# Kernel optimization log

Measured on AMD Instinct MI355X. Metric: run time of the kernel, lower is better.

Reference implementation:

```python
import jax, jax.numpy as jnp
import numpy as np

IMG = 224; P = 16; C_IN = 3; D = 768; DEPTH = 12; H = 12; HD = D // H
MLP = 4 * D; NCLS = 1000
GRID = IMG // P; NPATCH = GRID * GRID; N = NPATCH + 1
NRD = (2 * GRID - 1) * (2 * GRID - 1) + 3  # num_relative_distance


def _rel_pos_index():
    # replicates the torch buffer construction (BEiT-style)
    coords = np.stack(np.meshgrid(np.arange(GRID), np.arange(GRID), indexing='ij')).reshape(2, -1)
    rel = (coords[:, :, None] - coords[:, None, :]).transpose(1, 2, 0).astype(np.int64)
    rel[:, :, 0] += GRID - 1
    rel[:, :, 1] += GRID - 1
    rel[:, :, 0] *= 2 * GRID - 1
    idx = np.zeros((N, N), dtype=np.int64)
    idx[1:, 1:] = rel.sum(-1)
    idx[0, :] = NRD - 3
    idx[:, 0] = NRD - 2
    idx[0, 0] = NRD - 1
    return jnp.asarray(idx)

REL_IDX = _rel_pos_index()  # [N, N] int


def setup_inputs() -> dict:
    key = jax.random.key(0)
    ks = jax.random.split(key, 12)
    r = lambda k, shp: jax.random.normal(k, shp, jnp.float32) * 0.02
    return {
        'x': jax.random.normal(ks[0], (32, C_IN, IMG, IMG), jnp.float32),
        'patch_w': r(ks[1], (D, C_IN * P * P)),
        'patch_b': jnp.zeros((D,), jnp.float32),
        'cls_token': r(ks[2], (1, 1, D)),
        'pos_embed': r(ks[3], (1, N, D)),
        'norm1_s': jnp.ones((DEPTH, D), jnp.float32),
        'norm1_b': jnp.zeros((DEPTH, D), jnp.float32),
        'qkv_w': r(ks[4], (DEPTH, 3 * D, D)),
        'q_bias': jnp.zeros((DEPTH, D), jnp.float32),
        'v_bias': jnp.zeros((DEPTH, D), jnp.float32),
        'rpb_table': r(ks[5], (DEPTH, NRD, H)),
        'proj_w': r(ks[6], (DEPTH, D, D)),
        'proj_b': jnp.zeros((DEPTH, D), jnp.float32),
        'norm2_s': jnp.ones((DEPTH, D), jnp.float32),
        'norm2_b': jnp.zeros((DEPTH, D), jnp.float32),
        'fc1_w': r(ks[7], (DEPTH, MLP, D)),
        'fc1_b': jnp.zeros((DEPTH, MLP), jnp.float32),
        'fc2_w': r(ks[8], (DEPTH, D, MLP)),
        'fc2_b': jnp.zeros((DEPTH, D), jnp.float32),
        'gamma1': jnp.full((DEPTH, D), 0.1, jnp.float32),
        'gamma2': jnp.full((DEPTH, D), 0.1, jnp.float32),
        'normf_s': jnp.ones((D,), jnp.float32),
        'normf_b': jnp.zeros((D,), jnp.float32),
        'head_w': r(ks[9], (NCLS, D)),
        'head_b': jnp.zeros((NCLS,), jnp.float32),
    }


def _ln(x, s, b):
    m = jnp.mean(x, -1, keepdims=True)
    v = jnp.mean((x - m) ** 2, -1, keepdims=True)
    return (x - m) * jax.lax.rsqrt(v + 1e-5) * s + b


def reference(x, patch_w, patch_b, cls_token, pos_embed, norm1_s, norm1_b, qkv_w,
              q_bias, v_bias, rpb_table, proj_w, proj_b, norm2_s, norm2_b,
              fc1_w, fc1_b, fc2_w, fc2_b, gamma1, gamma2, normf_s, normf_b,
              head_w, head_b):
    B = x.shape[0]
    # Patch embed: stride=kernel conv == unfold + matmul
    t = x.reshape(B, C_IN, GRID, P, GRID, P).transpose(0, 2, 4, 1, 3, 5).reshape(B, NPATCH, C_IN * P * P)
    t = t @ patch_w.T + patch_b                                   # [B, 196, D]
    t = jnp.concatenate([jnp.broadcast_to(cls_token, (B, 1, D)), t], axis=1) + pos_embed
    scale = HD ** -0.5
    for i in range(DEPTH):
        h = _ln(t, norm1_s[i], norm1_b[i])
        qkv_b = jnp.concatenate([q_bias[i], jnp.zeros_like(q_bias[i]), v_bias[i]])
        qkv = (h @ qkv_w[i].T + qkv_b).reshape(B, N, 3, H, HD)
        q = qkv[:, :, 0].transpose(0, 2, 1, 3)                    # [B, H, N, HD]
        k = qkv[:, :, 1].transpose(0, 2, 1, 3)
        v = qkv[:, :, 2].transpose(0, 2, 1, 3)
        bias = rpb_table[i][REL_IDX].transpose(2, 0, 1)           # [H, N, N]
        attn = jax.nn.softmax(jnp.einsum('bhqd,bhkd->bhqk', q * scale, k) + bias[None], axis=-1)
        o = jnp.einsum('bhqk,bhkd->bhqd', attn, v).transpose(0, 2, 1, 3).reshape(B, N, D)
        t = t + gamma1[i] * (o @ proj_w[i].T + proj_b[i])
        h2 = _ln(t, norm2_s[i], norm2_b[i])
        m = jax.nn.gelu(h2 @ fc1_w[i].T + fc1_b[i], approximate=False) @ fc2_w[i].T + fc2_b[i]
        t = t + gamma2[i] * m
    t = _ln(t, normf_s, normf_b)
    return t[:, 0] @ head_w.T + head_b                            # [B, NCLS]
```

## Files before the change

### kernel.cpp

```cpp
#include <hip/hip_runtime.h>
#include <hip/hip_bf16.h>


typedef __hip_bfloat16 bf16s;
using bf16x8 = __attribute__((ext_vector_type(8))) __bf16;
using f32x4  = __attribute__((ext_vector_type(4))) float;

#define DEV static __device__ __forceinline__

DEV float b2f(bf16s x) { return __bfloat162float(x); }
DEV bf16s f2b(float x) { return __float2bfloat16(x); }

DEV void gload_lds16(const void* g, void* l) {
  __builtin_amdgcn_global_load_lds((const __attribute__((address_space(1))) void*)g,
                                   (__attribute__((address_space(3))) void*)l, 16, 0, 0);
}

constexpr int B_   = 32;
constexpr int H_   = 12;
constexpr int NTOK = 197;
constexpr int NPAD = 224;
constexpr int MVALP= 6272;
constexpr int MVAL = B_*NTOK;
constexpr int MROW = 6400;
constexpr int MLP_ = 3072;
constexpr int BH   = B_*H_;
constexpr int NRD  = 732;
constexpr int NNP  = 224*224;

constexpr size_t OFF_T   = 0;
constexpr size_t SZ_T    = (size_t)MROW*768*4;
constexpr size_t OFF_H   = OFF_T + SZ_T;
constexpr size_t SZ_H    = (size_t)MROW*768*2;
constexpr size_t OFF_Q   = OFF_H + SZ_H;
constexpr size_t SZ_QKB  = (size_t)BH*NPAD*64*2;
constexpr size_t OFF_K   = OFF_Q + SZ_QKB;
constexpr size_t OFF_VT  = OFF_K + SZ_QKB;
constexpr size_t OFF_P   = OFF_VT + SZ_QKB;
constexpr size_t SZ_P    = (size_t)MROW*MLP_*2;
constexpr size_t OFF_O   = OFF_P + SZ_P;
constexpr size_t OFF_BT  = OFF_O + SZ_H;
constexpr size_t SZ_BT   = (size_t)12*H_*NNP*2;
constexpr size_t OFF_HF  = OFF_BT + SZ_BT;
constexpr size_t OFF_WB  = OFF_HF + 49152;
constexpr size_t WS_NEED = OFF_WB + (size_t)7077888*2;

constexpr size_t WB_QKV = 0;
constexpr size_t WB_PROJ= (size_t)2304*768;
constexpr size_t WB_FC1 = WB_PROJ + (size_t)768*768;
constexpr size_t WB_FC2 = WB_FC1 + (size_t)MLP_*768;

template<int MODE>
__global__ __launch_bounds__(512, 4)
void gemm8p(const bf16s* __restrict__ A, const bf16s* __restrict__ Bw,
            const int K, const int ldc,
            bf16s* __restrict__ Cb,
            const float* __restrict__ e0, const float* __restrict__ e1,
            float* __restrict__ tres,
            bf16s* __restrict__ qp, bf16s* __restrict__ kp, bf16s* __restrict__ vp)
{
  __shared__ bf16s lds[32768];
  const int tid  = threadIdx.x;
  const int lane = tid & 63;
  const int wid  = tid >> 6;
  const int wm   = wid >> 2, wn = wid & 3;

  const int ncols = gridDim.y;
  const int nwg = (int)gridDim.x * ncols;
  const int lin = (int)blockIdx.y * gridDim.x + blockIdx.x;
  const int xcd = lin & 7, pos = lin >> 3;
  const int q8 = nwg >> 3, r8 = nwg & 7;
  const int vid = (xcd < r8) ? xcd*(q8+1) + pos : r8*(q8+1) + (xcd-r8)*q8 + pos;
  constexpr int NBG = (MODE == 0) ? 6 : 8;
  const int gsz = NBG * (int)gridDim.x;
  const int g   = vid / gsz;
  const int rr  = vid - g*gsz;
  const int bm  = rr / NBG;
  const int bn  = g*NBG + (rr - bm*NBG);

  const int srow = (wid << 3) + (lane >> 3);
  const int colg = (((lane & 7) ^ (srow & 7)) << 3);
  const bf16s* gA = A  + (size_t)(bm*128 + srow)*K + colg;
  const bf16s* gB = Bw + (size_t)(bn*128 + srow)*K + colg;
  const size_t rK64 = (size_t)64*K;

  const int r15  = lane & 15;
  const int colr = (lane >> 4) << 3;
  const int exor = (lane & 7) << 3;
  const int ardA = wm*4096 + r15*64;
  const int ardB = 8192 + (wn*32 + r15)*64;

  f32x4 acc[4][2] = {};
  const int J = K >> 7;

#define STGA(h, kt, dbuf) do { \
    const bf16s* _g = gA + (size_t)(h)*rK64 + (size_t)(kt)*64; \
    gload_lds16(_g, &lds[(dbuf)*16384 + (h)*4096 + wid*512 + lane*8]); } while(0)
#define STGB(h, kt, dbuf) do { \
    const bf16s* _g = gB + (size_t)(h)*rK64 + (size_t)(kt)*64; \
    gload_lds16(_g, &lds[(dbuf)*16384 + 8192 + (h)*4096 + wid*512 + lane*8]); } while(0)

  STGB(0,0,0); STGB(1,0,0);
  STGA(0,0,0); STGA(1,0,0);
  STGB(0,1,1); STGB(1,1,1);

  bf16x8 bfr[2][2];

  for (int j = 0; j < J; ++j) {
    const bool more = (j+1 < J);
#pragma unroll
    for (int p = 0; p < 4; ++p) {
      __builtin_amdgcn_sched_barrier(0);
      if (p == 0) {
        asm volatile("s_waitcnt vmcnt(2)" ::: "memory");
      } else if (p == 2) {
        if (j+1 == J) asm volatile("s_waitcnt vmcnt(0)" ::: "memory");
        else          asm volatile("s_waitcnt vmcnt(2)" ::: "memory");
      }
      __builtin_amdgcn_sched_barrier(0);
      __builtin_amdgcn_s_barrier();
      __builtin_amdgcn_sched_barrier(0);

      if (p == 0)      { STGA(0, 2*j+1, 1); STGA(1, 2*j+1, 1); }
      else if (p == 1) { if (more) { STGB(0, 2*j+2, 0); STGB(1, 2*j+2, 0); } }
      else if (p == 2) { if (more) { STGA(0, 2*j+2, 0); STGA(1, 2*j+2, 0); } }
      else             { if (more) { STGB(0, 2*j+3, 1); STGB(1, 2*j+3, 1); } }

      const int d = (p < 2) ? 0 : 1;
      const int dbase = d*16384;
      const int q0 = (p & 1) << 1;
      if ((p & 1) == 0) {
#pragma unroll
        for (int nf=0; nf<2; nf++)
#pragma unroll
          for (int kss=0; kss<2; kss++)
            bfr[nf][kss] = *(const bf16x8*)&lds[dbase + ardB + nf*1024 + (((kss<<5) + colr) ^ exor)];
      }
      bf16x8 a1[2][2];
#pragma unroll
      for (int qq=0; qq<2; qq++)
#pragma unroll
        for (int kss=0; kss<2; kss++)
          a1[qq][kss] = *(const bf16x8*)&lds[dbase + ardA + (q0+qq)*1024 + (((kss<<5) + colr) ^ exor)];
      __builtin_amdgcn_s_setprio(1);
#pragma unroll
      for (int qq=0; qq<2; qq++)
#pragma unroll
        for (int nf=0; nf<2; nf++)
#pragma unroll
          for (int kss=0; kss<2; kss++)
            acc[q0+qq][nf] = __builtin_amdgcn_mfma_f32_16x16x32_bf16(a1[qq][kss], bfr[nf][kss], acc[q0+qq][nf], 0, 0, 0);
      __builtin_amdgcn_s_setprio(0);
    }
  }
#undef STGA
#undef STGB

  const int crow0 = (lane >> 4) * 4;

  if (MODE == 5) {
    __syncthreads();
#pragma unroll
    for (int mf = 0; mf < 4; ++mf)
#pragma unroll
      for (int nf = 0; nf < 2; ++nf)
#pragma unroll
        for (int r = 0; r < 4; ++r) {
          const int lrow = wm*64 + mf*16 + crow0 + r;
          const int lcol = wn*32 + nf*16 + r15;
          const float xx = acc[mf][nf][r] + e0[bn*128 + lcol];
          lds[lrow*136 + lcol] = f2b(0.5f*xx*(1.0f + erff(xx*0.70710678118654752f)));
        }
    __syncthreads();
#pragma unroll
    for (int it = 0; it < 4; ++it) {
      const int sid = it*512 + tid;
      const int row = sid >> 4, cg = sid & 15;
      const int grow = bm*128 + row;
      *(uint4*)&Cb[(size_t)grow*ldc + bn*128 + cg*8] =
          *(const uint4*)&lds[row*136 + cg*8];
    }
    return;
  }

  if (MODE == 0 && bn >= 12) {
    float* lf = (float*)lds;
    __syncthreads();
#pragma unroll
    for (int mf = 0; mf < 4; ++mf)
#pragma unroll
      for (int nf = 0; nf < 2; ++nf)
#pragma unroll
        for (int r = 0; r < 4; ++r) {
          const int col = wn*32 + nf*16 + r15;
          const int row = wm*64 + mf*16 + crow0 + r;
          lf[col*128 + (row ^ (col & 31))] = acc[mf][nf][r];
        }
    __syncthreads();
    const int rem0 = bn*128 - 1536;
#pragma unroll
    for (int ci = 0; ci < 16; ++ci) {
      const int c = wid*16 + ci;
      const int rem = rem0 + c;
      const int hh = rem >> 6, dd = rem & 63;
      const float vb = e1[rem];
      bf16s* vrow = vp + ((size_t)hh*64 + dd)*NPAD;
#pragma unroll
      for (int hf2 = 0; hf2 < 2; ++hf2) {
        const int row = hf2*64 + lane;
        const int grow = bm*128 + row;
        if (grow < MVAL) {
          const int b2 = grow/197, ntok = grow - b2*197;
          vrow[(size_t)b2*H_*64*NPAD + ntok] = f2b(lf[c*128 + (row ^ (c & 31))] + vb);
        }
      }
    }
    return;
  }

  if (MODE == 0) {
    const bool isq = (bn < 6);
    __syncthreads();
#pragma unroll
    for (int mf = 0; mf < 4; ++mf)
#pragma unroll
      for (int nf = 0; nf < 2; ++nf)
#pragma unroll
        for (int r = 0; r < 4; ++r) {
          const int lrow = wm*64 + mf*16 + crow0 + r;
          const int lcol = wn*32 + nf*16 + r15;
          float v = acc[mf][nf][r];
          if (isq) v = (v + e0[bn*128 + lcol])*0.125f;
          lds[lrow*136 + lcol] = f2b(v);
        }
    __syncthreads();
    bf16s* outp = isq ? qp : kp;
#pragma unroll
    for (int it = 0; it < 4; ++it) {
      const int sid = it*512 + tid;
      const int row = sid >> 4, cg = sid & 15;
      const int grow = bm*128 + row;
      if (grow < MVAL) {
        const int bb_ = grow/197, ntok = grow - bb_*197;
        const int lcol = cg*8;
        const int rem = isq ? (bn*128 + lcol) : (bn*128 + lcol - 768);
        const int hh = rem >> 6, dd = rem & 63;
        *(uint4*)&outp[(((size_t)bb_*H_ + hh)*NPAD + ntok)*64 + dd] =
            *(const uint4*)&lds[row*136 + lcol];
      }
    }
  }
}

template<int MODE>
__global__ __launch_bounds__(256, 3)
void gemm64n(const bf16s* __restrict__ A, const bf16s* __restrict__ Bw,
             const int K, const int ldc, bf16s* __restrict__ Cb,
             const float* __restrict__ e0, const float* __restrict__ e1,
             float* __restrict__ tres)
{
  __shared__ bf16s lds[24576];
  const int tid  = threadIdx.x;
  const int lane = tid & 63;
  const int wid  = tid >> 6;
  const int wm   = wid >> 1, wn = wid & 1;

  const int ncols = gridDim.y;
  const int nwg = (int)gridDim.x * ncols;
  const int lin = (int)blockIdx.y * gridDim.x + blockIdx.x;
  const int xcd = lin & 7, pos = lin >> 3;
  const int q8 = nwg >> 3, r8 = nwg & 7;
  const int vid = (xcd < r8) ? xcd*(q8+1) + pos : r8*(q8+1) + (xcd-r8)*q8 + pos;
  const int bm = vid / ncols, bn = vid - bm*ncols;

  const int srow = tid >> 3;
  const int colg = (((tid & 7) ^ (srow & 7)) << 3);
  const bf16s* gA = A  + (size_t)(bm*128 + srow)*K + colg;
  const bf16s* gB = Bw + (size_t)(bn*64  + srow)*K + colg;
  const size_t rK32 = (size_t)32*K;

  const int r15  = lane & 15;
  const int colr = (lane >> 4) << 3;
  const int exor = (lane & 7) << 3;
  const int ardA = wm*4096 + r15*64;
  const int ardB = 8192 + (wn*32 + r15)*64;

  f32x4 acc[4][2] = {};
  const int J = K >> 7;

#define STGA2(h, kt, dbuf) do { \
    const bf16s* _g = gA + (size_t)(h)*rK32 + (size_t)(kt)*64; \
    gload_lds16(_g, &lds[(dbuf)*12288 + (h)*2048 + tid*8]); } while(0)
#define STGB2(h, kt, dbuf) do { \
    const bf16s* _g = gB + (size_t)(h)*rK32 + (size_t)(kt)*64; \
    gload_lds16(_g, &lds[(dbuf)*12288 + 8192 + (h)*2048 + tid*8]); } while(0)

  STGB2(0,0,0); STGB2(1,0,0);
  STGA2(0,0,0); STGA2(1,0,0); STGA2(2,0,0); STGA2(3,0,0);
  STGB2(0,1,1); STGB2(1,1,1);

  bf16x8 bfr[2][2];

  for (int j = 0; j < J; ++j) {
    const bool more = (j+1 < J);
#pragma unroll
    for (int p = 0; p < 4; ++p) {
      __builtin_amdgcn_sched_barrier(0);
      if (p == 0) {
        asm volatile("s_waitcnt vmcnt(2)" ::: "memory");
      } else if (p == 2) {
        if (j+1 == J) asm volatile("s_waitcnt vmcnt(0)" ::: "memory");
        else          asm volatile("s_waitcnt vmcnt(2)" ::: "memory");
      }
      __builtin_amdgcn_sched_barrier(0);
      __builtin_amdgcn_s_barrier();
      __builtin_amdgcn_sched_barrier(0);

      if (p == 0)      { STGA2(0, 2*j+1, 1); STGA2(1, 2*j+1, 1); STGA2(2, 2*j+1, 1); STGA2(3, 2*j+1, 1); }
      else if (p == 1) { if (more) { STGB2(0, 2*j+2, 0); STGB2(1, 2*j+2, 0); } }
      else if (p == 2) { if (more) { STGA2(0, 2*j+2, 0); STGA2(1, 2*j+2, 0); STGA2(2, 2*j+2, 0); STGA2(3, 2*j+2, 0); } }
      else             { if (more) { STGB2(0, 2*j+3, 1); STGB2(1, 2*j+3, 1); } }

      const int d = (p < 2) ? 0 : 1;
      const int dbase = d*12288;
      const int q0 = (p & 1) << 1;
      if ((p & 1) == 0) {
#pragma unroll
        for (int nf=0; nf<2; nf++)
#pragma unroll
          for (int kss=0; kss<2; kss++)
            bfr[nf][kss] = *(const bf16x8*)&lds[dbase + ardB + nf*1024 + (((kss<<5) + colr) ^ exor)];
      }
      bf16x8 a1[2][2];
#pragma unroll
      for (int qq=0; qq<2; qq++)
#pragma unroll
        for (int kss=0; kss<2; kss++)
          a1[qq][kss] = *(const bf16x8*)&lds[dbase + ardA + (q0+qq)*1024 + (((kss<<5) + colr) ^ exor)];
      __builtin_amdgcn_s_setprio(1);
#pragma unroll
      for (int qq=0; qq<2; qq++)
#pragma unroll
        for (int nf=0; nf<2; nf++)
#pragma unroll
          for (int kss=0; kss<2; kss++)
            acc[q0+qq][nf] = __builtin_amdgcn_mfma_f32_16x16x32_bf16(a1[qq][kss], bfr[nf][kss], acc[q0+qq][nf], 0, 0, 0);
      __builtin_amdgcn_s_setprio(0);
    }
  }
#undef STGA2
#undef STGB2

  const int crow0 = (lane >> 4) * 4;
#pragma unroll
  for (int mf = 0; mf < 4; ++mf) {
#pragma unroll
    for (int r = 0; r < 4; ++r) {
      const int grow = bm*128 + wm*64 + mf*16 + crow0 + r;
      {
        float* trow = tres + (size_t)grow*768;
#pragma unroll
        for (int nf = 0; nf < 2; ++nf) {
          const int gcol = bn*64 + wn*32 + nf*16 + r15;
          trow[gcol] += e1[gcol]*(acc[mf][nf][r] + e0[gcol]);
        }
      }
    }
  }
}

__global__ __launch_bounds__(256, 5)
void gemm64p(const bf16s* __restrict__ A, const bf16s* __restrict__ Bw,
             int K,
             const float* __restrict__ e0, const float* __restrict__ e1,
             float* __restrict__ tres)
{
  __shared__ bf16s As[2][64*32];
  __shared__ bf16s Bs[2][128*32];
  const int tid  = threadIdx.x;
  const int lane = tid & 63;
  const int wave = tid >> 6;

  const int ncols = gridDim.y;
  const int nwg = (int)gridDim.x * ncols;
  const int lin = (int)blockIdx.y * gridDim.x + blockIdx.x;
  const int xcd = lin & 7, pos = lin >> 3;
  const int q8 = nwg >> 3, r8 = nwg & 7;
  const int vid = (xcd < r8) ? xcd*(q8+1) + pos : r8*(q8+1) + (xcd-r8)*q8 + pos;
  const int bm = vid / ncols, bn = vid - bm*ncols;

  f32x4 acc[2][4] = {};

  const int sr4  = lane >> 2;
  const int scol = ((lane&3) ^ (sr4&3))*8;
  const bf16s* gA = A  + (size_t)(bm*64  + wave*16 + sr4)*K + scol;
  const bf16s* gB = Bw + (size_t)(bn*128 + wave*32 + sr4)*K + scol;
  const size_t b16 = (size_t)16*K;
  const int dA  = wave*512  + lane*8;
  const int dB0 = wave*1024 + lane*8, dB1 = dB0 + 512;

  const int fr  = lane & 15;
  const int rdk = (((lane>>4) ^ (lane&3)))*8;
  const int wr = wave >> 1, wc = wave & 1;
  const int abase = (wr*32 + fr)*32 + rdk;
  const int bbase = (wc*64 + fr)*32 + rdk;

  const int nk = K >> 5;
  gload_lds16(gA,       &As[0][dA]);
  gload_lds16(gB,       &Bs[0][dB0]);
  gload_lds16(gB + b16, &Bs[0][dB1]);

  int cur = 0;
  for (int kt = 0; kt < nk; ++kt) {
    __syncthreads();
    if (kt + 1 < nk) {
      const bf16s* ga = gA + (size_t)(kt+1)*32;
      const bf16s* gb = gB + (size_t)(kt+1)*32;
      gload_lds16(ga,       &As[cur^1][dA]);
      gload_lds16(gb,       &Bs[cur^1][dB0]);
      gload_lds16(gb + b16, &Bs[cur^1][dB1]);
    }
    bf16x8 af[2], bfr[4];
    af[0] = *(const bf16x8*)&As[cur][abase];
    af[1] = *(const bf16x8*)&As[cur][abase + 512];
#pragma unroll
    for (int n2=0;n2<4;n2++) bfr[n2] = *(const bf16x8*)&Bs[cur][bbase + n2*512];
#pragma unroll
    for (int m=0;m<2;m++)
#pragma unroll
      for (int n2=0;n2<4;n2++)
        acc[m][n2] = __builtin_amdgcn_mfma_f32_16x16x32_bf16(af[m], bfr[n2], acc[m][n2], 0, 0, 0);
    cur ^= 1;
  }

  const int crow0 = (lane>>4)*4;
#pragma unroll
  for (int m=0;m<2;m++) {
#pragma unroll
    for (int r=0;r<4;r++) {
      const int grow = bm*64 + wr*32 + m*16 + crow0 + r;
      if (grow >= MVALP) continue;
      const int bb_ = grow/196, p = grow - bb_*196;
      float* trow = tres + ((size_t)bb_*197 + 1 + p)*768;
      const float* prow = e1 + (size_t)(1+p)*768;
#pragma unroll
      for (int n2=0;n2<4;n2++) {
        const int gcol = bn*128 + wc*64 + n2*16 + fr;
        trow[gcol] = acc[m][n2][r] + e0[gcol] + prow[gcol];
      }
    }
  }
}

__global__ __launch_bounds__(256)
void f2b_k(const float* __restrict__ src, bf16s* __restrict__ dst, int n4)
{
  int id = blockIdx.x*256 + threadIdx.x;
  if (id >= n4) return;
  const float4 v = ((const float4*)src)[id];
  union { bf16s b[4]; uint2 u; } uu;
  uu.b[0] = f2b(v.x); uu.b[1] = f2b(v.y); uu.b[2] = f2b(v.z); uu.b[3] = f2b(v.w);
  ((uint2*)dst)[id] = uu.u;
}

__global__ __launch_bounds__(256)
void prep_k(const float* __restrict__ tin, const float* __restrict__ s,
            const float* __restrict__ b, bf16s* __restrict__ outp,
            const float* __restrict__ qw, const float* __restrict__ pw,
            const float* __restrict__ f1, const float* __restrict__ f2,
            bf16s* __restrict__ wb)
{
  const int tid = threadIdx.x;
  if (blockIdx.x < MVAL) {
    const int r = blockIdx.x;
    const float* xr = tin + (size_t)r*768;
    float v0 = xr[tid], v1 = xr[tid+256], v2 = xr[tid+512];
    float sum = v0+v1+v2;
#pragma unroll
    for (int off=32; off>=1; off>>=1) sum += __shfl_xor(sum, off, 64);
    __shared__ float red[8];
    const int wv = tid>>6, ln = tid&63;
    if (ln==0) red[wv] = sum;
    __syncthreads();
    const float mean = (red[0]+red[1]+red[2]+red[3]) * (1.0f/768.0f);
    const float d0=v0-mean, d1=v1-mean, d2=v2-mean;
    float sq = d0*d0 + d1*d1 + d2*d2;
#pragma unroll
    for (int off=32; off>=1; off>>=1) sq += __shfl_xor(sq, off, 64);
    if (ln==0) red[4+wv] = sq;
    __syncthreads();
    const float rs = rsqrtf((red[4]+red[5]+red[6]+red[7])*(1.0f/768.0f) + 1e-5f);
    bf16s* orow = outp + (size_t)r*768;
    orow[tid]     = f2b(d0*rs*s[tid]     + b[tid]);
    orow[tid+256] = f2b(d1*rs*s[tid+256] + b[tid+256]);
    orow[tid+512] = f2b(d2*rs*s[tid+512] + b[tid+512]);
  } else {
    int id = (blockIdx.x - MVAL)*256 + tid;
    const float* src; size_t dst; int loc;
    if (id < 442368)           { src = qw; loc = id;          dst = WB_QKV; }
    else if (id < 589824)      { src = pw; loc = id-442368;   dst = WB_PROJ; }
    else if (id < 1179648)     { src = f1; loc = id-589824;   dst = WB_FC1; }
    else                       { src = f2; loc = id-1179648;  dst = WB_FC2; }
    const float4 v = ((const float4*)src)[loc];
    union { bf16s bb[4]; uint2 u; } uu;
    uu.bb[0] = f2b(v.x); uu.bb[1] = f2b(v.y); uu.bb[2] = f2b(v.z); uu.bb[3] = f2b(v.w);
    ((uint2*)(wb + dst))[loc] = uu.u;
  }
}

__global__ __launch_bounds__(256)
void bias_all_k(const float* __restrict__ rpb, bf16s* __restrict__ biasT)
{
  int id = blockIdx.x*256 + threadIdx.x;
  if (id >= 12*H_*NNP) return;
  const int l   = id / (H_*NNP);
  const int r2  = id - l*(H_*NNP);
  const int hh  = r2 / NNP;
  const int rem = r2 - hh*NNP;
  int i = rem / 224, j = rem - i*224;
  if (i > 196) i = 196;
  if (j > 196) j = 196;
  int v;
  if (i==0 && j==0)      v = NRD-1;
  else if (i==0)         v = NRD-3;
  else if (j==0)         v = NRD-2;
  else {
    const int p = i-1, q = j-1;
    v = (p/14 - q/14 + 13)*27 + (p%14 - q%14 + 13);
  }
  biasT[id] = f2b(rpb[(size_t)l*NRD*H_ + v*H_ + hh]);
}

__global__ __launch_bounds__(256)
void im2col_k(const float* __restrict__ x, bf16s* __restrict__ pat)
{
  int id = blockIdx.x*256 + threadIdx.x;
  if (id >= MVALP*768) return;
  int col = id % 768;  int row = id / 768;
  int b = row / 196, p = row % 196;
  int gy = p / 14, gx = p % 14;
  int c = col >> 8, rem = col & 255, py = rem >> 4, px = rem & 15;
  pat[id] = f2b(x[ ((size_t)(b*3 + c)*224 + gy*16 + py)*224 + gx*16 + px ]);
}

__global__ __launch_bounds__(256)
void clspos_k(const float* __restrict__ cls, const float* __restrict__ pos, float* __restrict__ t)
{
  int id = blockIdx.x*256 + threadIdx.x;
  int d = id % 768, b = id / 768;
  t[(size_t)b*197*768 + d] = cls[d] + pos[d];
}

__global__ __launch_bounds__(256)
void ln_k(const float* __restrict__ tin, const float* __restrict__ s,
          const float* __restrict__ b, bf16s* __restrict__ outp, int instride)
{
  const int r = blockIdx.x, tid = threadIdx.x;
  const float* xr = tin + (size_t)r*instride;
  float v0 = xr[tid], v1 = xr[tid+256], v2 = xr[tid+512];
  float sum = v0+v1+v2;
#pragma unroll
  for (int off=32; off>=1; off>>=1) sum += __shfl_xor(sum, off, 64);
  __shared__ float red[8];
  const int wv = tid>>6, ln = tid&63;
  if (ln==0) red[wv] = sum;
  __syncthreads();
  const float mean = (red[0]+red[1]+red[2]+red[3]) * (1.0f/768.0f);
  const float d0=v0-mean, d1=v1-mean, d2=v2-mean;
  float sq = d0*d0 + d1*d1 + d2*d2;
#pragma unroll
  for (int off=32; off>=1; off>>=1) sq += __shfl_xor(sq, off, 64);
  if (ln==0) red[4+wv] = sq;
  __syncthreads();
  const float rs = rsqrtf((red[4]+red[5]+red[6]+red[7])*(1.0f/768.0f) + 1e-5f);
  bf16s* orow = outp + (size_t)r*768;
  orow[tid]     = f2b(d0*rs*s[tid]     + b[tid]);
  orow[tid+256] = f2b(d1*rs*s[tid+256] + b[tid+256]);
  orow[tid+512] = f2b(d2*rs*s[tid+512] + b[tid+512]);
}

__global__ __launch_bounds__(64)
void attn_fused(const bf16s* __restrict__ q, const bf16s* __restrict__ k,
                const bf16s* __restrict__ vT, const bf16s* __restrict__ biasT,
                bf16s* __restrict__ o)
{
  __shared__ bf16s Pl[32][232];
  const int gid = blockIdx.x;
  const int qt = gid % 7, bh = gid / 7;
  const int b = bh / H_, hh = bh % H_;
  const int lane = threadIdx.x;
  const int fr = lane & 15, fk = (lane>>4)*8;

  const bf16s* bTq = biasT + (size_t)hh*NNP + (size_t)(qt*32)*224;
#pragma unroll
  for (int rr = 0; rr < 32; ++rr) {
    if (lane < 28) gload_lds16(bTq + (size_t)rr*224 + lane*8, &Pl[rr][lane*8]);
  }

  const bf16s* qp = q + (size_t)bh*NPAD*64;
  const bf16s* kp = k + (size_t)bh*NPAD*64;
  bf16x8 a[2][2];
#pragma unroll
  for (int m=0;m<2;m++)
#pragma unroll
    for (int kk=0;kk<2;kk++)
      a[m][kk] = *(const bf16x8*)&qp[(qt*32 + m*16 + fr)*64 + kk*32 + fk];

  f32x4 acc[2][14] = {};
  __builtin_amdgcn_s_setprio(1);
#pragma unroll
  for (int nt=0; nt<14; nt++) {
    bf16x8 bb0 = *(const bf16x8*)&kp[(nt*16 + fr)*64 + fk];
    bf16x8 bb1 = *(const bf16x8*)&kp[(nt*16 + fr)*64 + 32 + fk];
    acc[0][nt] = __builtin_amdgcn_mfma_f32_16x16x32_bf16(a[0][0], bb0, acc[0][nt], 0,0,0);
    acc[0][nt] = __builtin_amdgcn_mfma_f32_16x16x32_bf16(a[0][1], bb1, acc[0][nt], 0,0,0);
    acc[1][nt] = __builtin_amdgcn_mfma_f32_16x16x32_bf16(a[1][0], bb0, acc[1][nt], 0,0,0);
    acc[1][nt] = __builtin_amdgcn_mfma_f32_16x16x32_bf16(a[1][1], bb1, acc[1][nt], 0,0,0);
  }
  __builtin_amdgcn_s_setprio(0);

  asm volatile("s_waitcnt vmcnt(0)" ::: "memory");
  __builtin_amdgcn_sched_barrier(0);

#pragma unroll
  for (int m=0;m<2;m++) {
#pragma unroll
    for (int r2=0;r2<4;r2++) {
      const int lrow = m*16 + (lane>>4)*4 + r2;
      const int row = qt*32 + lrow;
      if (row < NTOK) {
        float s[14]; float mx = -3.0e38f;
#pragma unroll
        for (int nt=0; nt<14; nt++) {
          const int col = nt*16 + fr;
          float v = acc[m][nt][r2] + ((col < NTOK) ? b2f(Pl[lrow][col]) : 0.0f);
          s[nt] = v;
          if (col < NTOK) mx = fmaxf(mx, v);
        }
        mx = fmaxf(mx, __shfl_xor(mx, 1, 64));
        mx = fmaxf(mx, __shfl_xor(mx, 2, 64));
        mx = fmaxf(mx, __shfl_xor(mx, 4, 64));
        mx = fmaxf(mx, __shfl_xor(mx, 8, 64));
        float sum = 0.f;
#pragma unroll
        for (int nt=0; nt<14; nt++) {
          const int col = nt*16 + fr;
          float p = (col < NTOK) ? __expf(s[nt]-mx) : 0.0f;
          s[nt] = p; sum += p;
        }
        sum += __shfl_xor(sum, 1, 64);
        sum += __shfl_xor(sum, 2, 64);
        sum += __shfl_xor(sum, 4, 64);
        sum += __shfl_xor(sum, 8, 64);
        const float inv = 1.0f / sum;
#pragma unroll
        for (int nt=0; nt<14; nt++)
          Pl[lrow][nt*16 + fr] = f2b(s[nt]*inv);
      } else {
#pragma unroll
        for (int nt=0; nt<14; nt++)
          Pl[lrow][nt*16 + fr] = f2b(0.0f);
      }
    }
  }

  __syncthreads();

  const bf16s* Vp = vT + (size_t)bh*64*NPAD;
  f32x4 pacc[2][4] = {};
  __builtin_amdgcn_s_setprio(1);
  for (int kt=0; kt<7; kt++) {
    bf16x8 a0 = *(const bf16x8*)&Pl[fr][kt*32 + fk];
    bf16x8 a1 = *(const bf16x8*)&Pl[16 + fr][kt*32 + fk];
#pragma unroll
    for (int nf=0;nf<4;nf++) {
      bf16x8 bb = *(const bf16x8*)&Vp[(size_t)(nf*16 + fr)*NPAD + kt*32 + fk];
      pacc[0][nf] = __builtin_amdgcn_mfma_f32_16x16x32_bf16(a0, bb, pacc[0][nf], 0,0,0);
      pacc[1][nf] = __builtin_amdgcn_mfma_f32_16x16x32_bf16(a1, bb, pacc[1][nf], 0,0,0);
    }
  }
  __builtin_amdgcn_s_setprio(0);

  __syncthreads();
#pragma unroll
  for (int m=0;m<2;m++)
#pragma unroll
    for (int nf=0;nf<4;nf++)
#pragma unroll
      for (int r2=0;r2<4;r2++)
        Pl[m*16 + (lane>>4)*4 + r2][nf*16 + fr] = f2b(pacc[m][nf][r2]);
  __syncthreads();
  bf16s* obase = o + ((size_t)b*NTOK + qt*32)*768 + hh*64;
#pragma unroll
  for (int it=0; it<8; ++it) {
    const int id = it*64 + lane;
    const int row = id >> 4, c4 = (id & 15)*4;
    if (qt*32 + row < NTOK) {
      union { bf16s bb[4]; uint2 u; } uu;
      uu.bb[0]=Pl[row][c4]; uu.bb[1]=Pl[row][c4+1]; uu.bb[2]=Pl[row][c4+2]; uu.bb[3]=Pl[row][c4+3];
      *(uint2*)&obase[(size_t)row*768 + c4] = uu.u;
    }
  }
}

__global__ __launch_bounds__(256)
void head_k(const bf16s* __restrict__ hf, const float* __restrict__ hw,
            const float* __restrict__ hb, float* __restrict__ outp)
{
  const int b = blockIdx.y;
  const int n = blockIdx.x*256 + threadIdx.x;
  __shared__ float xs[768];
  for (int i=threadIdx.x; i<768; i+=256) xs[i] = b2f(hf[b*768+i]);
  __syncthreads();
  if (n < 1000) {
    const float* wr = hw + (size_t)n*768;
    float acc2 = hb[n];
    for (int k2=0;k2<768;k2++) acc2 += xs[k2]*wr[k2];
    outp[b*1000 + n] = acc2;
  }
}

extern "C" void kernel_launch(void* const* d_in, const int* in_sizes, int n_in,
                              void* d_out, int out_size, void* d_ws, size_t ws_size,
                              hipStream_t stream)
{
  const float* x       = (const float*)d_in[0];
  const float* patch_w = (const float*)d_in[1];
  const float* patch_b = (const float*)d_in[2];
  const float* cls_tok = (const float*)d_in[3];
  const float* pos_emb = (const float*)d_in[4];
  const float* norm1_s = (const float*)d_in[5];
  const float* norm1_b = (const float*)d_in[6];
  const float* qkv_w   = (const float*)d_in[7];
  const float* q_bias  = (const float*)d_in[8];
  const float* v_bias  = (const float*)d_in[9];
  const float* rpb     = (const float*)d_in[10];
  const float* proj_w  = (const float*)d_in[11];
  const float* proj_b  = (const float*)d_in[12];
  const float* norm2_s = (const float*)d_in[13];
  const float* norm2_b = (const float*)d_in[14];
  const float* fc1_w   = (const float*)d_in[15];
  const float* fc1_b   = (const float*)d_in[16];
  const float* fc2_w   = (const float*)d_in[17];
  const float* fc2_b   = (const float*)d_in[18];
  const float* gamma1  = (const float*)d_in[19];
  const float* gamma2  = (const float*)d_in[20];
  const float* normf_s = (const float*)d_in[21];
  const float* normf_b = (const float*)d_in[22];
  const float* head_w  = (const float*)d_in[23];
  const float* head_b  = (const float*)d_in[24];
  float* out = (float*)d_out;

  char* w = (char*)d_ws;
  float* t    = (float*)(w + OFF_T);
  bf16s* h    = (bf16s*)(w + OFF_H);
  bf16s* qb   = (bf16s*)(w + OFF_Q);
  bf16s* kb   = (bf16s*)(w + OFF_K);
  bf16s* vT   = (bf16s*)(w + OFF_VT);
  bf16s* m1   = (bf16s*)(w + OFF_P);
  bf16s* pat  = (bf16s*)(w + OFF_P);
  bf16s* o    = (bf16s*)(w + OFF_O);
  bf16s* biasT= (bf16s*)(w + OFF_BT);
  bf16s* hf   = (bf16s*)(w + OFF_HF);
  bf16s* wb   = (bf16s*)(w + OFF_WB);
  (void)ws_size; (void)in_sizes; (void)n_in; (void)out_size; (void)WS_NEED;

  hipMemsetAsync(h  + (size_t)MVAL*768,  0, (size_t)(MROW-MVAL)*768*2,  stream);
  hipMemsetAsync(o  + (size_t)MVAL*768,  0, (size_t)(MROW-MVAL)*768*2,  stream);
  hipMemsetAsync(m1 + (size_t)MVAL*MLP_, 0, (size_t)(MROW-MVAL)*MLP_*2, stream);
  hipMemsetAsync(qb, 0, SZ_QKB, stream);
  hipMemsetAsync(kb, 0, SZ_QKB, stream);
  hipMemsetAsync(vT, 0, SZ_QKB, stream);

  bias_all_k<<<(12*H_*NNP + 255)/256, 256, 0, stream>>>(rpb, biasT);
  im2col_k<<<(MVALP*768)/256, 256, 0, stream>>>(x, pat);
  clspos_k<<<96, 256, 0, stream>>>(cls_tok, pos_emb, t);
  f2b_k<<<(768*768/4)/256, 256, 0, stream>>>(patch_w, wb, 768*768/4);
  gemm64p<<<dim3(98,6), 256, 0, stream>>>(pat, wb, 768, patch_b, pos_emb, t);

  for (int l = 0; l < 12; ++l) {
    prep_k<<<MVAL + 6912, 256, 0, stream>>>(t, norm1_s + l*768, norm1_b + l*768, h,
                                            qkv_w + (size_t)l*2304*768, proj_w + (size_t)l*768*768,
                                            fc1_w + (size_t)l*MLP_*768, fc2_w + (size_t)l*768*MLP_, wb);
    gemm8p<0><<<dim3(50,18), 512, 0, stream>>>(h, wb + WB_QKV, 768, 2304, nullptr,
                                               q_bias + l*768, v_bias + l*768, nullptr,
                                               qb, kb, vT);
    attn_fused<<<BH*7, 64, 0, stream>>>(qb, kb, vT, biasT + (size_t)l*H_*NNP, o);
    gemm64n<2><<<dim3(50,12), 256, 0, stream>>>(o, wb + WB_PROJ, 768, 0, nullptr,
                                                proj_b + l*768, gamma1 + l*768, t);
    ln_k<<<MVAL, 256, 0, stream>>>(t, norm2_s + l*768, norm2_b + l*768, h, 768);
    gemm8p<5><<<dim3(50,24), 512, 0, stream>>>(h, wb + WB_FC1, 768, MLP_, m1,
                                               fc1_b + l*MLP_, nullptr, nullptr,
                                               nullptr, nullptr, nullptr);
    gemm64n<4><<<dim3(50,12), 256, 0, stream>>>(m1, wb + WB_FC2, 3072, 0, nullptr,
                                                fc2_b + l*768, gamma2 + l*768, t);
  }

  ln_k<<<32, 256, 0, stream>>>(t, normf_s, normf_b, hf, 197*768);
  head_k<<<dim3(4,32), 256, 0, stream>>>(hf, head_w, head_b, out);
}
```

Before: 2.728 ms.

## Pre-permute attention bias into MFMA fragment order and skip padded key tile

The precomputed relative-position bias table is stored in a per-query-tile layout matching the MFMA accumulator fragment order, so each lane reads its bias values as packed 32-bit words instead of scattered bf16 loads, and the global-to-LDS copy becomes a contiguous 14-chunk load. The QK^T loop drops the 14th key tile, which covers only padding columns beyond 197, removing MFMAs and column-validity checks. Rows are processed m=1 first and bias words are read before the Pl buffer is overwritten in place. This relies on the packed layout being staged into the padded 232-wide LDS array without corrupting data still needed.

```diff
diff --git a/kernel.cpp b/kernel.cpp
--- a/kernel.cpp
+++ b/kernel.cpp
@@ -26,7 +26,7 @@
 constexpr int MLP_ = 3072;
 constexpr int BH   = B_*H_;
 constexpr int NRD  = 732;
-constexpr int NNP  = 224*224;
+constexpr int NNP  = 7*32*16*14;
 
 constexpr size_t OFF_T   = 0;
 constexpr size_t SZ_T    = (size_t)MROW*768*4;
@@ -517,7 +517,14 @@
   const int r2  = id - l*(H_*NNP);
   const int hh  = r2 / NNP;
   const int rem = r2 - hh*NNP;
-  int i = rem / 224, j = rem - i*224;
+  const int qt   = rem / 7168;
+  const int idx2 = rem - qt*7168;
+  const int lrow = idx2 / 224;
+  const int idx3 = idx2 - lrow*224;
+  const int fr   = idx3 / 14;
+  const int nt   = idx3 - fr*14;
+  int i = qt*32 + lrow;
+  int j = nt*16 + fr;
   if (i > 196) i = 196;
   if (j > 196) j = 196;
   int v;
@@ -585,17 +592,18 @@
                 bf16s* __restrict__ o)
 {
   __shared__ bf16s Pl[32][232];
+  bf16s* Plf = &Pl[0][0];
   const int gid = blockIdx.x;
   const int qt = gid % 7, bh = gid / 7;
   const int b = bh / H_, hh = bh % H_;
   const int lane = threadIdx.x;
   const int fr = lane & 15, fk = (lane>>4)*8;
-
-  const bf16s* bTq = biasT + (size_t)hh*NNP + (size_t)(qt*32)*224;
-#pragma unroll
-  for (int rr = 0; rr < 32; ++rr) {
-    if (lane < 28) gload_lds16(bTq + (size_t)rr*224 + lane*8, &Pl[rr][lane*8]);
-  }
+  const int g4 = (lane >> 4) * 4;
+
+  const bf16s* bTq = biasT + (size_t)hh*NNP + (size_t)qt*7168;
+#pragma unroll
+  for (int it = 0; it < 14; ++it)
+    gload_lds16(bTq + it*512 + lane*8, &Plf[it*512 + lane*8]);
 
   const bf16s* qp = q + (size_t)bh*NPAD*64;
   const bf16s* kp = k + (size_t)bh*NPAD*64;
@@ -606,10 +614,10 @@
     for (int kk=0;kk<2;kk++)
       a[m][kk] = *(const bf16x8*)&qp[(qt*32 + m*16 + fr)*64 + kk*32 + fk];
 
-  f32x4 acc[2][14] = {};
+  f32x4 acc[2][13] = {};
   __builtin_amdgcn_s_setprio(1);
 #pragma unroll
-  for (int nt=0; nt<14; nt++) {
+  for (int nt=0; nt<13; nt++) {
     bf16x8 bb0 = *(const bf16x8*)&kp[(nt*16 + fr)*64 + fk];
     bf16x8 bb1 = *(const bf16x8*)&kp[(nt*16 + fr)*64 + 32 + fk];
     acc[0][nt] = __builtin_amdgcn_mfma_f32_16x16x32_bf16(a[0][0], bb0, acc[0][nt], 0,0,0);
@@ -622,20 +630,39 @@
   asm volatile("s_waitcnt vmcnt(0)" ::: "memory");
   __builtin_amdgcn_sched_barrier(0);
 
-#pragma unroll
-  for (int m=0;m<2;m++) {
-#pragma unroll
-    for (int r2=0;r2<4;r2++) {
-      const int lrow = m*16 + (lane>>4)*4 + r2;
+  const uint* Plu = (const uint*)Plf;
+  const bf16s zb = f2b(0.0f);
+
+#pragma unroll
+  for (int mm = 0; mm < 2; ++mm) {
+    const int m = 1 - mm;
+    uint br[4][7];
+#pragma unroll
+    for (int r2 = 0; r2 < 4; ++r2) {
+      const int lrow = m*16 + g4 + r2;
+      const int ub = (lrow*224 + fr*14) >> 1;
+#pragma unroll
+      for (int j = 0; j < 7; ++j) br[r2][j] = Plu[ub + j];
+    }
+#pragma unroll
+    for (int r2 = 0; r2 < 4; ++r2) {
+      const int lrow = m*16 + g4 + r2;
       const int row = qt*32 + lrow;
       if (row < NTOK) {
-        float s[14]; float mx = -3.0e38f;
-#pragma unroll
-        for (int nt=0; nt<14; nt++) {
-          const int col = nt*16 + fr;
-          float v = acc[m][nt][r2] + ((col < NTOK) ? b2f(Pl[lrow][col]) : 0.0f);
+        float s[13]; float mx = -3.0e38f;
+#pragma unroll
+        for (int nt = 0; nt < 12; ++nt) {
+          const uint u = br[r2][nt >> 1];
+          const uint bb = (nt & 1) ? (u & 0xffff0000u) : (u << 16);
+          const float v = acc[m][nt][r2] + __uint_as_float(bb);
           s[nt] = v;
-          if (col < NTOK) mx = fmaxf(mx, v);
+          mx = fmaxf(mx, v);
+        }
+        {
+          const uint u = br[r2][6];
+          const float v = acc[m][12][r2] + __uint_as_float(u << 16);
+          s[12] = v;
+          if (fr < 5) mx = fmaxf(mx, v);
         }
         mx = fmaxf(mx, __shfl_xor(mx, 1, 64));
         mx = fmaxf(mx, __shfl_xor(mx, 2, 64));
@@ -643,10 +670,13 @@
         mx = fmaxf(mx, __shfl_xor(mx, 8, 64));
         float sum = 0.f;
 #pragma unroll
-        for (int nt=0; nt<14; nt++) {
-          const int col = nt*16 + fr;
-          float p = (col < NTOK) ? __expf(s[nt]-mx) : 0.0f;
+        for (int nt = 0; nt < 12; ++nt) {
+          const float p = __expf(s[nt] - mx);
           s[nt] = p; sum += p;
+        }
+        {
+          const float p = (fr < 5) ? __expf(s[12] - mx) : 0.0f;
+          s[12] = p; sum += p;
         }
         sum += __shfl_xor(sum, 1, 64);
         sum += __shfl_xor(sum, 2, 64);
@@ -654,12 +684,13 @@
         sum += __shfl_xor(sum, 8, 64);
         const float inv = 1.0f / sum;
 #pragma unroll
-        for (int nt=0; nt<14; nt++)
+        for (int nt = 0; nt < 13; ++nt)
           Pl[lrow][nt*16 + fr] = f2b(s[nt]*inv);
+        Pl[lrow][208 + fr] = zb;
       } else {
 #pragma unroll
-        for (int nt=0; nt<14; nt++)
-          Pl[lrow][nt*16 + fr] = f2b(0.0f);
+        for (int nt = 0; nt < 14; ++nt)
+          Pl[lrow][nt*16 + fr] = zb;
       }
     }
   }
```

Result: no change. 2.702 ms (-1.0%).
